# Kernel optimization log

Hardware: AMD Instinct MI355X
Metric: run time of the kernel (lower is better)

## Reference

```python
import jax, jax.numpy as jnp
import numpy as np

B, CLEN, QLEN, H = 16, 4096, 512, 256


def setup_inputs() -> dict:
    key = jax.random.key(0)
    ks = jax.random.split(key, 8)
    scale = 1.0 / np.sqrt(H)
    return {
        "c": jax.random.normal(ks[0], (B, CLEN, H), dtype=jnp.float32),
        "q": jax.random.normal(ks[1], (B, QLEN, H), dtype=jnp.float32),
        "w_c": jax.random.normal(ks[2], (H,), dtype=jnp.float32) * scale,
        "b_c": jax.random.normal(ks[3], (), dtype=jnp.float32) * scale,
        "w_q": jax.random.normal(ks[4], (H,), dtype=jnp.float32) * scale,
        "b_q": jax.random.normal(ks[5], (), dtype=jnp.float32) * scale,
        "w_cq": jax.random.normal(ks[6], (H,), dtype=jnp.float32) * scale,
        "b_cq": jax.random.normal(ks[7], (), dtype=jnp.float32) * scale,
    }


def reference(c, q, w_c, b_c, w_q, b_q, w_cq, b_cq):
    # Trilinear similarity: s[b,i,j] = c_i.w_c + q_j.w_q + sum_d w_cq[d]*c[b,i,d]*q[b,j,d] + biases
    cq = jnp.einsum("bid,bjd->bij", c * w_cq, q) + b_cq          # (B, c_len, q_len)
    s = (c @ w_c + b_c)[:, :, None] + (q @ w_q + b_q)[:, None, :] + cq
    # context-to-query attention
    a = jax.nn.softmax(s, axis=2)                                  # (B, c_len, q_len)
    c2q_att = jnp.einsum("bij,bjd->bid", a, q)                     # (B, c_len, H)
    # query-to-context attention (max over queries, softmax over context)
    b_att = jax.nn.softmax(jnp.max(s, axis=2), axis=1)             # (B, c_len)
    q2c_att = jnp.einsum("bi,bid->bd", b_att, c)[:, None, :]       # (B, 1, H)
    q2c_att = jnp.broadcast_to(q2c_att, c.shape)                   # (B, c_len, H)
    x = jnp.concatenate([c, c2q_att, c * c2q_att, c * q2c_att], axis=2)
    return x  # (B, c_len, 4*H)
```

## Files before the change

### kernel.cpp

```cpp
#include <hip/hip_runtime.h>
#include <hip/hip_fp16.h>

constexpr int NB = 16;
constexpr int CL = 4096;
constexpr int QL = 512;
constexpr int HD = 256;

typedef _Float16 f16x8 __attribute__((ext_vector_type(8)));
typedef _Float16 f16x4 __attribute__((ext_vector_type(4)));
typedef float    f32x4 __attribute__((ext_vector_type(4)));


__global__ void k_prep_q(const float* __restrict__ q, const float* __restrict__ w_q,
                         const float* __restrict__ b_q, const float* __restrict__ w_cq,
                         const float* __restrict__ b_cq,
                         _Float16* __restrict__ qph, float* __restrict__ qd2) {
    int row  = blockIdx.x * 4 + (threadIdx.x >> 6);
    int lane = threadIdx.x & 63;
    float4 qv  = ((const float4*)(q + (size_t)row * HD))[lane];
    float4 wq  = ((const float4*)w_q)[lane];
    float4 wcq = ((const float4*)w_cq)[lane];
    f16x4 hv = {(_Float16)(qv.x * wcq.x), (_Float16)(qv.y * wcq.y),
                (_Float16)(qv.z * wcq.z), (_Float16)(qv.w * wcq.w)};
    *(f16x4*)(qph + (size_t)row * HD + lane * 4) = hv;
    float s = qv.x * wq.x + qv.y * wq.y + qv.z * wq.z + qv.w * wq.w;
    #pragma unroll
    for (int off = 32; off; off >>= 1) s += __shfl_down(s, off, 64);
    if (lane == 0) qd2[row] = s + b_q[0] + b_cq[0];
}

__global__ void k_cdot(const float* __restrict__ c, const float* __restrict__ w_c,
                       const float* __restrict__ b_c, float* __restrict__ cdot) {
    int row  = blockIdx.x * 4 + (threadIdx.x >> 6);
    int lane = threadIdx.x & 63;
    float4 cv = ((const float4*)(c + (size_t)row * HD))[lane];
    float4 wv = ((const float4*)w_c)[lane];
    float s = cv.x * wv.x + cv.y * wv.y + cv.z * wv.z + cv.w * wv.w;
    #pragma unroll
    for (int off = 32; off; off >>= 1) s += __shfl_down(s, off, 64);
    if (lane == 0) cdot[row] = s + b_c[0];
}

__global__ void k_tq(const float* __restrict__ q, _Float16* __restrict__ qth) {
    __shared__ float tile[64][65];
    int b  = blockIdx.z;
    int d0 = blockIdx.x * 64;
    int j0 = blockIdx.y * 64;
    int t  = threadIdx.x;
    int rr = t >> 4, cseg = t & 15;
    #pragma unroll
    for (int p = 0; p < 4; ++p) {
        int r = rr + p * 16;
        float4 v = *(const float4*)(q + ((size_t)b * QL + j0 + r) * HD + d0 + cseg * 4);
        tile[r][cseg * 4 + 0] = v.x; tile[r][cseg * 4 + 1] = v.y;
        tile[r][cseg * 4 + 2] = v.z; tile[r][cseg * 4 + 3] = v.w;
    }
    __syncthreads();
    #pragma unroll
    for (int p = 0; p < 4; ++p) {
        int dr = rr + p * 16;
        f16x4 hv = {(_Float16)tile[cseg * 4 + 0][dr], (_Float16)tile[cseg * 4 + 1][dr],
                    (_Float16)tile[cseg * 4 + 2][dr], (_Float16)tile[cseg * 4 + 3][dr]};
        *(f16x4*)(qth + ((size_t)b * HD + d0 + dr) * QL + j0 + cseg * 4) = hv;
    }
}

__launch_bounds__(256)
__global__ void k_gemm1(const float* __restrict__ c, const _Float16* __restrict__ qph,
                        const float* __restrict__ qd2, _Float16* __restrict__ sp) {
    __shared__ _Float16 As[128][72];
    __shared__ _Float16 Bs[128][72];
    const int b  = blockIdx.z;
    const int i0 = blockIdx.y * 128;
    const int j0 = blockIdx.x * 128;
    const int t  = threadIdx.x;
    const int wave = t >> 6, wi = wave >> 1, wj = wave & 1;
    const int ln = t & 15, quad = (t >> 4) & 3;
    f32x4 acc[4][4];
    #pragma unroll
    for (int a = 0; a < 4; ++a)
        #pragma unroll
        for (int bb = 0; bb < 4; ++bb) acc[a][bb] = (f32x4){0.f, 0.f, 0.f, 0.f};

    for (int dc = 0; dc < 4; ++dc) {
        __syncthreads();
        #pragma unroll
        for (int p = 0; p < 4; ++p) {
            int idx = t + p * 256;
            int row = idx >> 3, g = idx & 7;
            const float* src = c + ((size_t)b * CL + i0 + row) * HD + dc * 64 + g * 8;
            float4 v0 = *(const float4*)src;
            float4 v1 = *(const float4*)(src + 4);
            f16x8 hv = {(_Float16)v0.x, (_Float16)v0.y, (_Float16)v0.z, (_Float16)v0.w,
                        (_Float16)v1.x, (_Float16)v1.y, (_Float16)v1.z, (_Float16)v1.w};
            *(f16x8*)&As[row][g * 8] = hv;
        }
        #pragma unroll
        for (int p = 0; p < 4; ++p) {
            int idx = t + p * 256;
            int row = idx >> 3, g = idx & 7;
            f16x8 hv = *(const f16x8*)(qph + ((size_t)b * QL + j0 + row) * HD + dc * 64 + g * 8);
            *(f16x8*)&Bs[row][g * 8] = hv;
        }
        __syncthreads();
        #pragma unroll
        for (int ks = 0; ks < 2; ++ks) {
            f16x8 af[4], bf[4];
            #pragma unroll
            for (int it = 0; it < 4; ++it)
                af[it] = *(const f16x8*)&As[wi * 64 + it * 16 + ln][ks * 32 + quad * 8];
            #pragma unroll
            for (int jt = 0; jt < 4; ++jt)
                bf[jt] = *(const f16x8*)&Bs[wj * 64 + jt * 16 + ln][ks * 32 + quad * 8];
            #pragma unroll
            for (int it = 0; it < 4; ++it)
                #pragma unroll
                for (int jt = 0; jt < 4; ++jt)
                    acc[it][jt] = __builtin_amdgcn_mfma_f32_16x16x32_f16(af[it], bf[jt], acc[it][jt], 0, 0, 0);
        }
    }
    float qdv[4];
    #pragma unroll
    for (int jt = 0; jt < 4; ++jt) qdv[jt] = qd2[b * QL + j0 + wj * 64 + jt * 16 + ln];
    #pragma unroll
    for (int it = 0; it < 4; ++it)
        #pragma unroll
        for (int r = 0; r < 4; ++r) {
            int i = i0 + wi * 64 + it * 16 + quad * 4 + r;
            _Float16* dst = sp + ((size_t)b * CL + i) * QL + j0 + wj * 64 + ln;
            #pragma unroll
            for (int jt = 0; jt < 4; ++jt)
                dst[jt * 16] = (_Float16)(acc[it][jt][r] + qdv[jt]);
        }
}

__global__ void k_softmax(__half* __restrict__ sp, float* __restrict__ rowmax) {
    int row  = blockIdx.x * 4 + (threadIdx.x >> 6);
    int lane = threadIdx.x & 63;
    float4* rp = (float4*)(sp + (size_t)row * QL);
    union { float4 f; __half h[8]; } u;
    u.f = rp[lane];
    float v[8];
    #pragma unroll
    for (int k = 0; k < 8; ++k) v[k] = __half2float(u.h[k]);
    float m = v[0];
    #pragma unroll
    for (int k = 1; k < 8; ++k) m = fmaxf(m, v[k]);
    #pragma unroll
    for (int off = 32; off; off >>= 1) m = fmaxf(m, __shfl_xor(m, off, 64));
    float l = 0.f;
    #pragma unroll
    for (int k = 0; k < 8; ++k) { v[k] = __expf(v[k] - m); l += v[k]; }
    #pragma unroll
    for (int off = 32; off; off >>= 1) l += __shfl_xor(l, off, 64);
    float inv = 1.0f / l;
    #pragma unroll
    for (int k = 0; k < 8; ++k) u.h[k] = __float2half(v[k] * inv);
    rp[lane] = u.f;
    if (lane == 0) rowmax[row] = m;
}

__global__ void k_batch_mz(const float* __restrict__ rowmax, const float* __restrict__ cdot,
                           float* __restrict__ Mb, float* __restrict__ Zb,
                           float* __restrict__ q2c) {
    int b = blockIdx.x, t = threadIdx.x;
    q2c[b * HD + t] = 0.f;
    float vals[16];
    float m = -1e30f;
    #pragma unroll
    for (int k = 0; k < 16; ++k) {
        int i = t + k * 256;
        vals[k] = rowmax[b * CL + i] + cdot[b * CL + i];
        m = fmaxf(m, vals[k]);
    }
    __shared__ float redm[4], redz[4];
    #pragma unroll
    for (int off = 32; off; off >>= 1) m = fmaxf(m, __shfl_xor(m, off, 64));
    if ((t & 63) == 0) redm[t >> 6] = m;
    __syncthreads();
    m = fmaxf(fmaxf(redm[0], redm[1]), fmaxf(redm[2], redm[3]));
    float z = 0.f;
    #pragma unroll
    for (int k = 0; k < 16; ++k) z += __expf(vals[k] - m);
    #pragma unroll
    for (int off = 32; off; off >>= 1) z += __shfl_xor(z, off, 64);
    if ((t & 63) == 0) redz[t >> 6] = z;
    __syncthreads();
    if (t == 0) { Mb[b] = m; Zb[b] = redz[0] + redz[1] + redz[2] + redz[3]; }
}

__global__ void k_q2c(const float* __restrict__ c, const float* __restrict__ rowmax,
                      const float* __restrict__ cdot, const float* __restrict__ Mb,
                      const float* __restrict__ Zb, float* __restrict__ q2c) {
    int b = blockIdx.x >> 6, slab = blockIdx.x & 63;
    int dd = threadIdx.x;
    float M = Mb[b], invZ = 1.0f / Zb[b];
    float acc = 0.f;
    for (int r = 0; r < 64; ++r) {
        int i = slab * 64 + r;
        float w = __expf(rowmax[b * CL + i] + cdot[b * CL + i] - M);
        acc += w * c[((size_t)b * CL + i) * HD + dd];
    }
    atomicAdd(&q2c[b * HD + dd], acc * invZ);
}

__launch_bounds__(256)
__global__ void k_gemm2(const float* __restrict__ c, const _Float16* __restrict__ sp,
                        const _Float16* __restrict__ qth, const float* __restrict__ q2c,
                        float* __restrict__ x) {
    __shared__ _Float16 As[128][72];
    __shared__ _Float16 Bs[128][72];
    const int b  = blockIdx.z;
    const int i0 = blockIdx.y * 128;
    const int d0 = blockIdx.x * 128;
    const int t  = threadIdx.x;
    const int wave = t >> 6, wi = wave >> 1, wj = wave & 1;
    const int ln = t & 15, quad = (t >> 4) & 3;
    f32x4 acc[4][4];
    #pragma unroll
    for (int a = 0; a < 4; ++a)
        #pragma unroll
        for (int bb = 0; bb < 4; ++bb) acc[a][bb] = (f32x4){0.f, 0.f, 0.f, 0.f};

    for (int jc = 0; jc < 8; ++jc) {
        __syncthreads();
        #pragma unroll
        for (int p = 0; p < 4; ++p) {
            int idx = t + p * 256;
            int row = idx >> 3, g = idx & 7;
            f16x8 hv = *(const f16x8*)(sp + ((size_t)b * CL + i0 + row) * QL + jc * 64 + g * 8);
            *(f16x8*)&As[row][g * 8] = hv;
        }
        #pragma unroll
        for (int p = 0; p < 4; ++p) {
            int idx = t + p * 256;
            int row = idx >> 3, g = idx & 7;
            f16x8 hv = *(const f16x8*)(qth + ((size_t)b * HD + d0 + row) * QL + jc * 64 + g * 8);
            *(f16x8*)&Bs[row][g * 8] = hv;
        }
        __syncthreads();
        #pragma unroll
        for (int ks = 0; ks < 2; ++ks) {
            f16x8 af[4], bf[4];
            #pragma unroll
            for (int it = 0; it < 4; ++it)
                af[it] = *(const f16x8*)&As[wi * 64 + it * 16 + ln][ks * 32 + quad * 8];
            #pragma unroll
            for (int jt = 0; jt < 4; ++jt)
                bf[jt] = *(const f16x8*)&Bs[wj * 64 + jt * 16 + ln][ks * 32 + quad * 8];
            #pragma unroll
            for (int it = 0; it < 4; ++it)
                #pragma unroll
                for (int jt = 0; jt < 4; ++jt)
                    acc[it][jt] = __builtin_amdgcn_mfma_f32_16x16x32_f16(af[it], bf[jt], acc[it][jt], 0, 0, 0);
        }
    }
    float q2cv[4];
    #pragma unroll
    for (int jt = 0; jt < 4; ++jt) q2cv[jt] = q2c[b * HD + d0 + wj * 64 + jt * 16 + ln];
    #pragma unroll
    for (int it = 0; it < 4; ++it)
        #pragma unroll
        for (int r = 0; r < 4; ++r) {
            int i = i0 + wi * 64 + it * 16 + quad * 4 + r;
            const float* crow = c + ((size_t)b * CL + i) * HD;
            float* xrow = x + ((size_t)b * CL + i) * (4 * HD);
            #pragma unroll
            for (int jt = 0; jt < 4; ++jt) {
                int d = d0 + wj * 64 + jt * 16 + ln;
                float cv = crow[d];
                float a  = acc[it][jt][r];
                xrow[d]          = cv;
                xrow[HD + d]     = a;
                xrow[2 * HD + d] = cv * a;
                xrow[3 * HD + d] = cv * q2cv[jt];
            }
        }
}

extern "C" void kernel_launch(void* const* d_in, const int* in_sizes, int n_in,
                              void* d_out, int out_size, void* d_ws, size_t ws_size,
                              hipStream_t stream) {
    const float* c    = (const float*)d_in[0];
    const float* q    = (const float*)d_in[1];
    const float* w_c  = (const float*)d_in[2];
    const float* b_c  = (const float*)d_in[3];
    const float* w_q  = (const float*)d_in[4];
    const float* b_q  = (const float*)d_in[5];
    const float* w_cq = (const float*)d_in[6];
    const float* b_cq = (const float*)d_in[7];
    float* x = (float*)d_out;

    char* ws = (char*)d_ws;
    _Float16* qph  = (_Float16*)(ws);
    _Float16* qth  = (_Float16*)(ws + 4194304);
    float*  qd2    = (float*)(ws + 8388608);
    float*  cdot   = (float*)(ws + 8421376);
    float*  rowmax = (float*)(ws + 8683520);
    float*  Mb     = (float*)(ws + 8945664);
    float*  Zb     = (float*)(ws + 8945728);
    float*  q2c    = (float*)(ws + 8945792);
    _Float16* sp   = (_Float16*)(ws + 8962176);

    k_prep_q<<<NB * QL / 4, 256, 0, stream>>>(q, w_q, b_q, w_cq, b_cq, qph, qd2);
    k_cdot<<<NB * CL / 4, 256, 0, stream>>>(c, w_c, b_c, cdot);
    k_tq<<<dim3(HD / 64, QL / 64, NB), 256, 0, stream>>>(q, qth);
    k_gemm1<<<dim3(QL / 128, CL / 128, NB), 256, 0, stream>>>(c, qph, qd2, sp);
    k_softmax<<<NB * CL / 4, 256, 0, stream>>>((__half*)sp, rowmax);
    k_batch_mz<<<NB, 256, 0, stream>>>(rowmax, cdot, Mb, Zb, q2c);
    k_q2c<<<NB * 64, 256, 0, stream>>>(c, rowmax, cdot, Mb, Zb, q2c);
    k_gemm2<<<dim3(HD / 128, CL / 128, NB), 256, 0, stream>>>(c, sp, qth, q2c, x);
}
```

Measured before the change: 470.1 us.

## Fuse similarity GEMM, softmax and attention GEMM into one flash-style kernel

Replaces the gemm1, softmax and gemm2 kernels with one fused kernel. Each block computes a 64-row strip of the full 512-wide score matrix in registers, does the row softmax with cross-wave reductions in shared memory, writes the normalized probabilities to swizzled LDS, and runs the second GEMM against the transposed q directly from global memory. This removes the fp16 score matrix round trip through HBM and two kernel launches. The c-copy and c*q2c output columns move to a separate elementwise kernel. In exchange, the second GEMM's B operand is read uncached from global by every block, 64 KB of LDS per block limits occupancy, and the c columns are now read twice.

Result: slower. 490.1 us (+4.3%).

```diff
diff --git a/kernel.cpp b/kernel.cpp
--- a/kernel.cpp
+++ b/kernel.cpp
@@ -65,99 +65,202 @@
     }
 }
 
-__launch_bounds__(256)
-__global__ void k_gemm1(const float* __restrict__ c, const _Float16* __restrict__ qph,
-                        const float* __restrict__ qd2, _Float16* __restrict__ sp) {
-    __shared__ _Float16 As[128][72];
-    __shared__ _Float16 Bs[128][72];
-    const int b  = blockIdx.z;
-    const int i0 = blockIdx.y * 128;
-    const int j0 = blockIdx.x * 128;
+__launch_bounds__(512, 4)
+__global__ void k_fused(const float* __restrict__ c, const _Float16* __restrict__ qph,
+                        const float* __restrict__ qd2, const _Float16* __restrict__ qth,
+                        float* __restrict__ rowmax, float* __restrict__ x) {
+    __shared__ __align__(1024) char smem[65536];
+
+    const int b  = blockIdx.y;
+    const int i0 = blockIdx.x * 64;
     const int t  = threadIdx.x;
-    const int wave = t >> 6, wi = wave >> 1, wj = wave & 1;
-    const int ln = t & 15, quad = (t >> 4) & 3;
+    const int wave = t >> 6;
+    const int ln   = t & 15;
+    const int quad = (t >> 4) & 3;
+    const int jw   = wave;
+
     f32x4 acc[4][4];
     #pragma unroll
-    for (int a = 0; a < 4; ++a)
-        #pragma unroll
-        for (int bb = 0; bb < 4; ++bb) acc[a][bb] = (f32x4){0.f, 0.f, 0.f, 0.f};
+    for (int mt = 0; mt < 4; ++mt)
+        #pragma unroll
+        for (int nt = 0; nt < 4; ++nt) acc[mt][nt] = (f32x4){0.f, 0.f, 0.f, 0.f};
 
     for (int dc = 0; dc < 4; ++dc) {
         __syncthreads();
-        #pragma unroll
-        for (int p = 0; p < 4; ++p) {
-            int idx = t + p * 256;
-            int row = idx >> 3, g = idx & 7;
-            const float* src = c + ((size_t)b * CL + i0 + row) * HD + dc * 64 + g * 8;
-            float4 v0 = *(const float4*)src;
-            float4 v1 = *(const float4*)(src + 4);
-            f16x8 hv = {(_Float16)v0.x, (_Float16)v0.y, (_Float16)v0.z, (_Float16)v0.w,
-                        (_Float16)v1.x, (_Float16)v1.y, (_Float16)v1.z, (_Float16)v1.w};
-            *(f16x8*)&As[row][g * 8] = hv;
-        }
-        #pragma unroll
-        for (int p = 0; p < 4; ++p) {
-            int idx = t + p * 256;
-            int row = idx >> 3, g = idx & 7;
-            f16x8 hv = *(const f16x8*)(qph + ((size_t)b * QL + j0 + row) * HD + dc * 64 + g * 8);
-            *(f16x8*)&Bs[row][g * 8] = hv;
+        {
+            const int row = t >> 3, seg = t & 7;
+            #pragma unroll
+            for (int p = 0; p < 8; ++p) {
+                int j = row + p * 64;
+                f16x8 hv = *(const f16x8*)(qph + ((size_t)b * QL + j) * HD + dc * 64 + seg * 8);
+                int byte = (j << 7) + (seg << 4);
+                byte ^= (j & 7) << 4;
+                *(f16x8*)(smem + byte) = hv;
+            }
         }
         __syncthreads();
         #pragma unroll
         for (int ks = 0; ks < 2; ++ks) {
-            f16x8 af[4], bf[4];
-            #pragma unroll
-            for (int it = 0; it < 4; ++it)
-                af[it] = *(const f16x8*)&As[wi * 64 + it * 16 + ln][ks * 32 + quad * 8];
-            #pragma unroll
-            for (int jt = 0; jt < 4; ++jt)
-                bf[jt] = *(const f16x8*)&Bs[wj * 64 + jt * 16 + ln][ks * 32 + quad * 8];
-            #pragma unroll
-            for (int it = 0; it < 4; ++it)
+            f16x8 bf[4];
+            #pragma unroll
+            for (int nt = 0; nt < 4; ++nt) {
+                const float* src = c + ((size_t)b * CL + i0 + nt * 16 + ln) * HD
+                                     + dc * 64 + ks * 32 + quad * 8;
+                float4 v0 = *(const float4*)src;
+                float4 v1 = *(const float4*)(src + 4);
+                bf[nt] = (f16x8){(_Float16)v0.x, (_Float16)v0.y, (_Float16)v0.z, (_Float16)v0.w,
+                                 (_Float16)v1.x, (_Float16)v1.y, (_Float16)v1.z, (_Float16)v1.w};
+            }
+            #pragma unroll
+            for (int mt = 0; mt < 4; ++mt) {
+                int j = jw * 64 + mt * 16 + ln;
+                int byte = (j << 7) + (ks * 64 + quad * 16);
+                byte ^= (j & 7) << 4;
+                f16x8 af = *(const f16x8*)(smem + byte);
                 #pragma unroll
-                for (int jt = 0; jt < 4; ++jt)
-                    acc[it][jt] = __builtin_amdgcn_mfma_f32_16x16x32_f16(af[it], bf[jt], acc[it][jt], 0, 0, 0);
-        }
-    }
-    float qdv[4];
-    #pragma unroll
-    for (int jt = 0; jt < 4; ++jt) qdv[jt] = qd2[b * QL + j0 + wj * 64 + jt * 16 + ln];
-    #pragma unroll
-    for (int it = 0; it < 4; ++it)
+                for (int nt = 0; nt < 4; ++nt)
+                    acc[mt][nt] = __builtin_amdgcn_mfma_f32_16x16x32_f16(af, bf[nt], acc[mt][nt], 0, 0, 0);
+            }
+        }
+    }
+
+    float m[4];
+    #pragma unroll
+    for (int nt = 0; nt < 4; ++nt) m[nt] = -1e30f;
+    #pragma unroll
+    for (int mt = 0; mt < 4; ++mt) {
+        float4 qv = *(const float4*)(qd2 + b * QL + jw * 64 + mt * 16 + quad * 4);
+        #pragma unroll
+        for (int nt = 0; nt < 4; ++nt) {
+            acc[mt][nt][0] += qv.x; acc[mt][nt][1] += qv.y;
+            acc[mt][nt][2] += qv.z; acc[mt][nt][3] += qv.w;
+            m[nt] = fmaxf(m[nt], fmaxf(fmaxf(acc[mt][nt][0], acc[mt][nt][1]),
+                                       fmaxf(acc[mt][nt][2], acc[mt][nt][3])));
+        }
+    }
+    #pragma unroll
+    for (int nt = 0; nt < 4; ++nt) {
+        m[nt] = fmaxf(m[nt], __shfl_xor(m[nt], 16, 64));
+        m[nt] = fmaxf(m[nt], __shfl_xor(m[nt], 32, 64));
+    }
+    __syncthreads();
+    float* redM = (float*)smem;
+    float* redZ = (float*)(smem + 2048);
+    if (quad == 0) {
+        #pragma unroll
+        for (int nt = 0; nt < 4; ++nt) redM[jw * 64 + nt * 16 + ln] = m[nt];
+    }
+    __syncthreads();
+    #pragma unroll
+    for (int nt = 0; nt < 4; ++nt) {
+        int ri = nt * 16 + ln;
+        float mm = redM[ri];
+        #pragma unroll
+        for (int w = 1; w < 8; ++w) mm = fmaxf(mm, redM[w * 64 + ri]);
+        m[nt] = mm;
+    }
+    if (jw == 0 && quad == 0) {
+        #pragma unroll
+        for (int nt = 0; nt < 4; ++nt)
+            rowmax[(size_t)b * CL + i0 + nt * 16 + ln] = m[nt];
+    }
+    float z[4] = {0.f, 0.f, 0.f, 0.f};
+    #pragma unroll
+    for (int mt = 0; mt < 4; ++mt)
+        #pragma unroll
+        for (int nt = 0; nt < 4; ++nt) {
+            #pragma unroll
+            for (int r = 0; r < 4; ++r) {
+                float e = __expf(acc[mt][nt][r] - m[nt]);
+                acc[mt][nt][r] = e;
+                z[nt] += e;
+            }
+        }
+    #pragma unroll
+    for (int nt = 0; nt < 4; ++nt) {
+        z[nt] += __shfl_xor(z[nt], 16, 64);
+        z[nt] += __shfl_xor(z[nt], 32, 64);
+    }
+    if (quad == 0) {
+        #pragma unroll
+        for (int nt = 0; nt < 4; ++nt) redZ[jw * 64 + nt * 16 + ln] = z[nt];
+    }
+    __syncthreads();
+    float inv[4];
+    #pragma unroll
+    for (int nt = 0; nt < 4; ++nt) {
+        int ri = nt * 16 + ln;
+        float zz = redZ[ri];
+        #pragma unroll
+        for (int w = 1; w < 8; ++w) zz += redZ[w * 64 + ri];
+        inv[nt] = 1.0f / zz;
+    }
+    __syncthreads();
+
+    #pragma unroll
+    for (int mt = 0; mt < 4; ++mt) {
+        int jcol = jw * 64 + mt * 16 + quad * 4;
+        #pragma unroll
+        for (int nt = 0; nt < 4; ++nt) {
+            int i = nt * 16 + ln;
+            f16x4 hv = {(_Float16)(acc[mt][nt][0] * inv[nt]),
+                        (_Float16)(acc[mt][nt][1] * inv[nt]),
+                        (_Float16)(acc[mt][nt][2] * inv[nt]),
+                        (_Float16)(acc[mt][nt][3] * inv[nt])};
+            int byte = (i << 10) + (jcol << 1);
+            byte ^= (i & 7) << 4;
+            *(f16x4*)(smem + byte) = hv;
+        }
+    }
+    __syncthreads();
+
+    const int iw = wave >> 2;
+    const int dw = wave & 3;
+    f32x4 acc2[2][4];
+    #pragma unroll
+    for (int it = 0; it < 2; ++it)
+        #pragma unroll
+        for (int dt = 0; dt < 4; ++dt) acc2[it][dt] = (f32x4){0.f, 0.f, 0.f, 0.f};
+
+    const _Float16* qthb = qth + (size_t)b * HD * QL;
+    #pragma unroll 4
+    for (int kc = 0; kc < 16; ++kc) {
+        f16x8 af[2], bf[4];
+        #pragma unroll
+        for (int it = 0; it < 2; ++it) {
+            int i = iw * 32 + it * 16 + ln;
+            int byte = (i << 10) + (kc * 64 + quad * 16);
+            byte ^= (i & 7) << 4;
+            af[it] = *(const f16x8*)(smem + byte);
+        }
+        #pragma unroll
+        for (int dt = 0; dt < 4; ++dt)
+            bf[dt] = *(const f16x8*)(qthb + (size_t)(dw * 64 + dt * 16 + ln) * QL
+                                     + kc * 32 + quad * 8);
+        #pragma unroll
+        for (int it = 0; it < 2; ++it)
+            #pragma unroll
+            for (int dt = 0; dt < 4; ++dt)
+                acc2[it][dt] = __builtin_amdgcn_mfma_f32_16x16x32_f16(af[it], bf[dt], acc2[it][dt], 0, 0, 0);
+    }
+
+    #pragma unroll
+    for (int it = 0; it < 2; ++it) {
         #pragma unroll
         for (int r = 0; r < 4; ++r) {
-            int i = i0 + wi * 64 + it * 16 + quad * 4 + r;
-            _Float16* dst = sp + ((size_t)b * CL + i) * QL + j0 + wj * 64 + ln;
-            #pragma unroll
-            for (int jt = 0; jt < 4; ++jt)
-                dst[jt * 16] = (_Float16)(acc[it][jt][r] + qdv[jt]);
-        }
-}
-
-__global__ void k_softmax(__half* __restrict__ sp, float* __restrict__ rowmax) {
-    int row  = blockIdx.x * 4 + (threadIdx.x >> 6);
-    int lane = threadIdx.x & 63;
-    float4* rp = (float4*)(sp + (size_t)row * QL);
-    union { float4 f; __half h[8]; } u;
-    u.f = rp[lane];
-    float v[8];
-    #pragma unroll
-    for (int k = 0; k < 8; ++k) v[k] = __half2float(u.h[k]);
-    float m = v[0];
-    #pragma unroll
-    for (int k = 1; k < 8; ++k) m = fmaxf(m, v[k]);
-    #pragma unroll
-    for (int off = 32; off; off >>= 1) m = fmaxf(m, __shfl_xor(m, off, 64));
-    float l = 0.f;
-    #pragma unroll
-    for (int k = 0; k < 8; ++k) { v[k] = __expf(v[k] - m); l += v[k]; }
-    #pragma unroll
-    for (int off = 32; off; off >>= 1) l += __shfl_xor(l, off, 64);
-    float inv = 1.0f / l;
-    #pragma unroll
-    for (int k = 0; k < 8; ++k) u.h[k] = __float2half(v[k] * inv);
-    rp[lane] = u.f;
-    if (lane == 0) rowmax[row] = m;
+            int i = i0 + iw * 32 + it * 16 + quad * 4 + r;
+            const float* crow = c + ((size_t)b * CL + i) * HD;
+            float* xrow = x + ((size_t)b * CL + i) * (4 * HD);
+            #pragma unroll
+            for (int dt = 0; dt < 4; ++dt) {
+                int d = dw * 64 + dt * 16 + ln;
+                float cv = crow[d];
+                float a  = acc2[it][dt][r];
+                xrow[HD + d]     = a;
+                xrow[2 * HD + d] = cv * a;
+            }
+        }
+    }
 }
 
 __global__ void k_batch_mz(const float* __restrict__ rowmax, const float* __restrict__ cdot,
@@ -204,78 +307,17 @@
     atomicAdd(&q2c[b * HD + dd], acc * invZ);
 }
 
-__launch_bounds__(256)
-__global__ void k_gemm2(const float* __restrict__ c, const _Float16* __restrict__ sp,
-                        const _Float16* __restrict__ qth, const float* __restrict__ q2c,
-                        float* __restrict__ x) {
-    __shared__ _Float16 As[128][72];
-    __shared__ _Float16 Bs[128][72];
-    const int b  = blockIdx.z;
-    const int i0 = blockIdx.y * 128;
-    const int d0 = blockIdx.x * 128;
-    const int t  = threadIdx.x;
-    const int wave = t >> 6, wi = wave >> 1, wj = wave & 1;
-    const int ln = t & 15, quad = (t >> 4) & 3;
-    f32x4 acc[4][4];
-    #pragma unroll
-    for (int a = 0; a < 4; ++a)
-        #pragma unroll
-        for (int bb = 0; bb < 4; ++bb) acc[a][bb] = (f32x4){0.f, 0.f, 0.f, 0.f};
-
-    for (int jc = 0; jc < 8; ++jc) {
-        __syncthreads();
-        #pragma unroll
-        for (int p = 0; p < 4; ++p) {
-            int idx = t + p * 256;
-            int row = idx >> 3, g = idx & 7;
-            f16x8 hv = *(const f16x8*)(sp + ((size_t)b * CL + i0 + row) * QL + jc * 64 + g * 8);
-            *(f16x8*)&As[row][g * 8] = hv;
-        }
-        #pragma unroll
-        for (int p = 0; p < 4; ++p) {
-            int idx = t + p * 256;
-            int row = idx >> 3, g = idx & 7;
-            f16x8 hv = *(const f16x8*)(qth + ((size_t)b * HD + d0 + row) * QL + jc * 64 + g * 8);
-            *(f16x8*)&Bs[row][g * 8] = hv;
-        }
-        __syncthreads();
-        #pragma unroll
-        for (int ks = 0; ks < 2; ++ks) {
-            f16x8 af[4], bf[4];
-            #pragma unroll
-            for (int it = 0; it < 4; ++it)
-                af[it] = *(const f16x8*)&As[wi * 64 + it * 16 + ln][ks * 32 + quad * 8];
-            #pragma unroll
-            for (int jt = 0; jt < 4; ++jt)
-                bf[jt] = *(const f16x8*)&Bs[wj * 64 + jt * 16 + ln][ks * 32 + quad * 8];
-            #pragma unroll
-            for (int it = 0; it < 4; ++it)
-                #pragma unroll
-                for (int jt = 0; jt < 4; ++jt)
-                    acc[it][jt] = __builtin_amdgcn_mfma_f32_16x16x32_f16(af[it], bf[jt], acc[it][jt], 0, 0, 0);
-        }
-    }
-    float q2cv[4];
-    #pragma unroll
-    for (int jt = 0; jt < 4; ++jt) q2cv[jt] = q2c[b * HD + d0 + wj * 64 + jt * 16 + ln];
-    #pragma unroll
-    for (int it = 0; it < 4; ++it)
-        #pragma unroll
-        for (int r = 0; r < 4; ++r) {
-            int i = i0 + wi * 64 + it * 16 + quad * 4 + r;
-            const float* crow = c + ((size_t)b * CL + i) * HD;
-            float* xrow = x + ((size_t)b * CL + i) * (4 * HD);
-            #pragma unroll
-            for (int jt = 0; jt < 4; ++jt) {
-                int d = d0 + wj * 64 + jt * 16 + ln;
-                float cv = crow[d];
-                float a  = acc[it][jt][r];
-                xrow[d]          = cv;
-                xrow[HD + d]     = a;
-                xrow[2 * HD + d] = cv * a;
-                xrow[3 * HD + d] = cv * q2cv[jt];
-            }
-        }
+__global__ void k_x03(const float* __restrict__ c, const float* __restrict__ q2c,
+                      float* __restrict__ x) {
+    int row  = blockIdx.x * 4 + (threadIdx.x >> 6);
+    int lane = threadIdx.x & 63;
+    int b = row >> 12;
+    float4 cv = ((const float4*)(c + (size_t)row * HD))[lane];
+    float4 qv = ((const float4*)(q2c + b * HD))[lane];
+    float4 o  = {cv.x * qv.x, cv.y * qv.y, cv.z * qv.z, cv.w * qv.w};
+    float* xrow = x + (size_t)row * (4 * HD);
+    ((float4*)xrow)[lane]            = cv;
+    ((float4*)(xrow + 3 * HD))[lane] = o;
 }
 
 extern "C" void kernel_launch(void* const* d_in, const int* in_sizes, int n_in,
@@ -300,14 +342,12 @@
     float*  Mb     = (float*)(ws + 8945664);
     float*  Zb     = (float*)(ws + 8945728);
     float*  q2c    = (float*)(ws + 8945792);
-    _Float16* sp   = (_Float16*)(ws + 8962176);
 
     k_prep_q<<<NB * QL / 4, 256, 0, stream>>>(q, w_q, b_q, w_cq, b_cq, qph, qd2);
     k_cdot<<<NB * CL / 4, 256, 0, stream>>>(c, w_c, b_c, cdot);
     k_tq<<<dim3(HD / 64, QL / 64, NB), 256, 0, stream>>>(q, qth);
-    k_gemm1<<<dim3(QL / 128, CL / 128, NB), 256, 0, stream>>>(c, qph, qd2, sp);
-    k_softmax<<<NB * CL / 4, 256, 0, stream>>>((__half*)sp, rowmax);
+    k_fused<<<dim3(CL / 64, NB), 512, 0, stream>>>(c, qph, qd2, qth, rowmax, x);
     k_batch_mz<<<NB, 256, 0, stream>>>(rowmax, cdot, Mb, Zb, q2c);
     k_q2c<<<NB * 64, 256, 0, stream>>>(c, rowmax, cdot, Mb, Zb, q2c);
-    k_gemm2<<<dim3(HD / 128, CL / 128, NB), 256, 0, stream>>>(c, sp, qth, q2c, x);
-}
+    k_x03<<<NB * CL / 4, 256, 0, stream>>>(c, q2c, x);
+}
```
